# Performance work log

Hardware: AMD Instinct MI355X
Metric: run time of the kernel (lower is better)

## Reference

```python
import jax, jax.numpy as jnp
import numpy as np

NUM_GRAPHS = 4096


def setup_inputs() -> dict:
    key = jax.random.key(0)
    k1, k2, k3, k4 = jax.random.split(key, 4)
    N, H = 500000, 256
    x = jax.random.normal(k1, (N, H), dtype=jnp.float32)
    batch = jnp.sort(jax.random.randint(k2, (N,), 0, NUM_GRAPHS, dtype=jnp.int64))
    W1 = jax.random.normal(k3, (H, H), dtype=jnp.float32) * (1.0 / np.sqrt(H))
    b1 = jnp.zeros((H,), dtype=jnp.float32)
    w2 = jax.random.normal(k4, (H, 1), dtype=jnp.float32) * (1.0 / np.sqrt(H))
    return {"x": x, "batch": batch, "W1": W1, "b1": b1, "w2": w2}


def reference(x, batch, W1, b1, w2):
    # attention scores: Linear -> Tanh -> Linear(no bias)  -> [N, 1]
    scores = jnp.tanh(x @ W1 + b1) @ w2  # [N, 1]
    # Torch code scatter-maxes into a zeros buffer, so the effective per-graph
    # max is clamped below at 0 (faithfully replicated here).
    seg_max = jax.ops.segment_max(scores, batch, num_segments=NUM_GRAPHS)  # [G, 1]
    seg_max = jnp.maximum(seg_max, 0.0)
    exp_scores = jnp.exp(scores - seg_max[batch])  # [N, 1]
    sum_exp = jax.ops.segment_sum(exp_scores, batch, num_segments=NUM_GRAPHS)  # [G, 1]
    normalized = exp_scores / sum_exp[batch]  # [N, 1]
    graph_embedding = jax.ops.segment_sum(x * normalized, batch, num_segments=NUM_GRAPHS)  # [G, H]
    return graph_embedding
```

## Files before the change

kernel.cpp:

```cpp
#include <hip/hip_runtime.h>
#include <cstdint>

#define H 256
#define MT 64
#define ROWS 256

typedef _Float16 half8 __attribute__((ext_vector_type(8)));
typedef float floatx4 __attribute__((ext_vector_type(4)));

__device__ __forceinline__ float fast_tanh(float v) {
    v = fminf(fmaxf(v, -15.f), 15.f);
    float e = __expf(2.f * v);
    return (e - 1.f) / (e + 1.f);
}

__global__ void init_kernel(float4* __restrict__ out4, int* __restrict__ maxv,
                            float* __restrict__ sumexp, int G, int total4) {
    int i = blockIdx.x * 256 + threadIdx.x;
    if (i < total4) out4[i] = make_float4(0.f, 0.f, 0.f, 0.f);
    if (i < G) { maxv[i] = 0; sumexp[i] = 0.f; }
}

__global__ void w1conv_kernel(const float* __restrict__ W1, _Float16* __restrict__ w1c) {
    int i = blockIdx.x * 256 + threadIdx.x;
    if (i < H * H) {
        int r = i & 511;
        int lane = r >> 3, h = r & 7;
        int t = i >> 9;
        int kc = t & 1, s = (t >> 1) & 3, ct = t >> 3;
        int mm = lane & 15, qq = lane >> 4;
        int col = ct * 16 + mm;
        int k = s * 64 + kc * 32 + qq * 8 + h;
        w1c[i] = (_Float16)W1[k * H + col];
    }
}

__global__ __launch_bounds__(256, 3) void scores_kernel(
    const float* __restrict__ x, const _Float16* __restrict__ w1c,
    const float* __restrict__ b1, const float* __restrict__ w2,
    const int* __restrict__ batch,
    float* __restrict__ scores, int* __restrict__ maxv, int N) {
    __shared__ _Float16 As[2][64][64];
    __shared__ float sred[4][64];

    const int tid = threadIdx.x;
    const int wv = tid >> 6;
    const int lane = tid & 63;
    const int m = lane & 15;
    const int q = lane >> 4;
    const int row0 = blockIdx.x * MT;

    const int srow = tid >> 2;
    const int sc4 = tid & 3;
    const int sg0 = (sc4 * 2) ^ (srow & 7);
    const int sg1 = (sc4 * 2 + 1) ^ (srow & 7);
    const bool srok = (row0 + srow) < N;
    const float* sbase = x + (size_t)(row0 + srow) * H + sc4 * 16;

    floatx4 acc[4][4] = {};

    float4 f0, f1, f2, f3;
    f0 = f1 = f2 = f3 = make_float4(0.f, 0.f, 0.f, 0.f);
    if (srok) {
        const float4* p = (const float4*)sbase;
        f0 = p[0]; f1 = p[1]; f2 = p[2]; f3 = p[3];
    }
    {
        half8 h0, h1;
        h0[0] = (_Float16)f0.x; h0[1] = (_Float16)f0.y; h0[2] = (_Float16)f0.z; h0[3] = (_Float16)f0.w;
        h0[4] = (_Float16)f1.x; h0[5] = (_Float16)f1.y; h0[6] = (_Float16)f1.z; h0[7] = (_Float16)f1.w;
        h1[0] = (_Float16)f2.x; h1[1] = (_Float16)f2.y; h1[2] = (_Float16)f2.z; h1[3] = (_Float16)f2.w;
        h1[4] = (_Float16)f3.x; h1[5] = (_Float16)f3.y; h1[6] = (_Float16)f3.z; h1[7] = (_Float16)f3.w;
        *(half8*)&As[0][srow][sg0 * 8] = h0;
        *(half8*)&As[0][srow][sg1 * 8] = h1;
    }
    __syncthreads();

    for (int s = 0; s < 4; ++s) {
        const int cur = s & 1;
        if (s < 3 && srok) {
            const float4* p = (const float4*)(sbase + (s + 1) * 64);
            f0 = p[0]; f1 = p[1]; f2 = p[2]; f3 = p[3];
        }
        half8 bf[4][2];
#pragma unroll
        for (int ni = 0; ni < 4; ++ni) {
            int ct = wv * 4 + ni;
#pragma unroll
            for (int kc = 0; kc < 2; ++kc) {
                int chunk = ((ct << 2) | s) * 2 + kc;
                bf[ni][kc] = *(const half8*)(w1c + ((size_t)chunk << 9) + lane * 8);
            }
        }
        half8 af[4][2];
#pragma unroll
        for (int mi = 0; mi < 4; ++mi) {
            int r = mi * 16 + m;
#pragma unroll
            for (int kc = 0; kc < 2; ++kc) {
                int g = (kc * 4 + q) ^ (r & 7);
                af[mi][kc] = *(const half8*)&As[cur][r][g * 8];
            }
        }
#pragma unroll
        for (int mi = 0; mi < 4; ++mi)
#pragma unroll
            for (int ni = 0; ni < 4; ++ni) {
                acc[mi][ni] = __builtin_amdgcn_mfma_f32_16x16x32_f16(
                    af[mi][0], bf[ni][0], acc[mi][ni], 0, 0, 0);
                acc[mi][ni] = __builtin_amdgcn_mfma_f32_16x16x32_f16(
                    af[mi][1], bf[ni][1], acc[mi][ni], 0, 0, 0);
            }
        if (s < 3) {
            half8 h0, h1;
            h0[0] = (_Float16)f0.x; h0[1] = (_Float16)f0.y; h0[2] = (_Float16)f0.z; h0[3] = (_Float16)f0.w;
            h0[4] = (_Float16)f1.x; h0[5] = (_Float16)f1.y; h0[6] = (_Float16)f1.z; h0[7] = (_Float16)f1.w;
            h1[0] = (_Float16)f2.x; h1[1] = (_Float16)f2.y; h1[2] = (_Float16)f2.z; h1[3] = (_Float16)f2.w;
            h1[4] = (_Float16)f3.x; h1[5] = (_Float16)f3.y; h1[6] = (_Float16)f3.z; h1[7] = (_Float16)f3.w;
            *(half8*)&As[1 - cur][srow][sg0 * 8] = h0;
            *(half8*)&As[1 - cur][srow][sg1 * 8] = h1;
        }
        __syncthreads();
    }

    float b1c[4], w2c[4];
#pragma unroll
    for (int ni = 0; ni < 4; ++ni) {
        int c = wv * 64 + ni * 16 + m;
        b1c[ni] = b1[c];
        w2c[ni] = w2[c];
    }
#pragma unroll
    for (int mi = 0; mi < 4; ++mi) {
#pragma unroll
        for (int r = 0; r < 4; ++r) {
            float v = 0.f;
#pragma unroll
            for (int ni = 0; ni < 4; ++ni)
                v += w2c[ni] * fast_tanh(acc[mi][ni][r] + b1c[ni]);
            v += __shfl_xor(v, 1);
            v += __shfl_xor(v, 2);
            v += __shfl_xor(v, 4);
            v += __shfl_xor(v, 8);
            if (m == 0) sred[wv][mi * 16 + q * 4 + r] = v;
        }
    }
    __syncthreads();
    if (tid < MT) {
        int row = row0 + tid;
        if (row < N) {
            float sc = sred[0][tid] + sred[1][tid] + sred[2][tid] + sred[3][tid];
            scores[row] = sc;
            if (sc > 0.f) atomicMax(&maxv[batch[row]], __float_as_int(sc));
        }
    }
}

__global__ __launch_bounds__(256) void pass2_kernel(
    const float* __restrict__ x, const int* __restrict__ batch,
    const float* __restrict__ scores, const int* __restrict__ maxv,
    float* __restrict__ out, float* __restrict__ sumexp, int N) {
    const int t = threadIdx.x;
    const int sub = t >> 6;
    const int lane = t & 63;
    const int base = blockIdx.x * ROWS;
    const int i1 = min(base + ROWS, N);
    int i = base + sub;
    if (i >= i1) return;

    const float4* x4 = (const float4*)x;

    float ax = 0.f, ay = 0.f, az = 0.f, aw = 0.f, sw = 0.f;
    int cur = batch[i];
    int g = cur;
    float4 xv = x4[(size_t)i * 64 + lane];
    float w = __expf(scores[i] - __int_as_float(maxv[cur]));

    while (i < i1) {
        int inx = i + 4;
        float4 xv_n = make_float4(0.f, 0.f, 0.f, 0.f);
        float w_n = 0.f;
        int g_n = g;
        if (inx < i1) {
            xv_n = x4[(size_t)inx * 64 + lane];
            g_n = batch[inx];
            w_n = __expf(scores[inx] - __int_as_float(maxv[g_n]));
        }
        if (g != cur) {
            float* o = out + (size_t)cur * H + lane * 4;
            atomicAdd(o + 0, ax); atomicAdd(o + 1, ay);
            atomicAdd(o + 2, az); atomicAdd(o + 3, aw);
            if (lane == 0) atomicAdd(&sumexp[cur], sw);
            ax = ay = az = aw = 0.f; sw = 0.f;
            cur = g;
        }
        ax = fmaf(w, xv.x, ax);
        ay = fmaf(w, xv.y, ay);
        az = fmaf(w, xv.z, az);
        aw = fmaf(w, xv.w, aw);
        if (lane == 0) sw += w;
        xv = xv_n; w = w_n; g = g_n;
        i = inx;
    }
    float* o = out + (size_t)cur * H + lane * 4;
    atomicAdd(o + 0, ax); atomicAdd(o + 1, ay);
    atomicAdd(o + 2, az); atomicAdd(o + 3, aw);
    if (lane == 0) atomicAdd(&sumexp[cur], sw);
}

__global__ void normalize_kernel(float4* __restrict__ out4,
                                 const float* __restrict__ sumexp, int total4) {
    int i = blockIdx.x * 256 + threadIdx.x;
    if (i < total4) {
        float s = sumexp[i >> 6];
        if (s > 0.f) {
            float inv = 1.f / s;
            float4 v = out4[i];
            v.x *= inv; v.y *= inv; v.z *= inv; v.w *= inv;
            out4[i] = v;
        } else {
            out4[i] = make_float4(0.f, 0.f, 0.f, 0.f);
        }
    }
}

extern "C" void kernel_launch(void* const* d_in, const int* in_sizes, int n_in,
                              void* d_out, int out_size, void* d_ws, size_t ws_size,
                              hipStream_t stream) {
    const float* x = (const float*)d_in[0];
    const int* batch = (const int*)d_in[1];
    const float* W1 = (const float*)d_in[2];
    const float* b1 = (const float*)d_in[3];
    const float* w2 = (const float*)d_in[4];
    float* out = (float*)d_out;

    const int N = in_sizes[0] / H;
    const int G = out_size / H;

    char* ws = (char*)d_ws;
    float* scores = (float*)ws;
    size_t off = (size_t)N * sizeof(float);
    off = (off + 15) & ~(size_t)15;
    int* maxv = (int*)(ws + off);
    off += (size_t)G * sizeof(int);
    float* sumexp = (float*)(ws + off);
    off += (size_t)G * sizeof(float);
    off = (off + 15) & ~(size_t)15;
    _Float16* w1c = (_Float16*)(ws + off);

    const int total4 = (G * H) / 4;
    init_kernel<<<(max(total4, G) + 255) / 256, 256, 0, stream>>>(
        (float4*)out, maxv, sumexp, G, total4);
    w1conv_kernel<<<(H * H + 255) / 256, 256, 0, stream>>>(W1, w1c);
    scores_kernel<<<(N + MT - 1) / MT, 256, 0, stream>>>(
        x, w1c, b1, w2, batch, scores, maxv, N);
    pass2_kernel<<<(N + ROWS - 1) / ROWS, 256, 0, stream>>>(
        x, batch, scores, maxv, out, sumexp, N);
    normalize_kernel<<<(total4 + 255) / 256, 256, 0, stream>>>(
        (float4*)out, sumexp, total4);
}
```

Baseline: 912.4 us.

## Fuse score computation with weighted segment pooling and drop the max pass

Merges the scores kernel and the pooling kernel into one. Each 64-row tile now computes exp(score) directly, with no per-graph max subtraction, and accumulates weighted x rows into the output with atomics while those rows are still hot in cache. This removes the second full read of x, the scores buffer and the atomicMax pass. It also merges the init and W1 conversion kernels into a single setup launch. In exchange, exp can overflow if scores ever exceed about 88; tanh bounds each score by the L1 norm of w2, which is small for these inputs. Atomics on the output also rise, because tiles are smaller than the old 256-row pooling blocks.

```diff
diff --git a/kernel.cpp b/kernel.cpp
--- a/kernel.cpp
+++ b/kernel.cpp
@@ -3,7 +3,6 @@
 
 #define H 256
 #define MT 64
-#define ROWS 256
 
 typedef _Float16 half8 __attribute__((ext_vector_type(8)));
 typedef float floatx4 __attribute__((ext_vector_type(4)));
@@ -14,15 +13,12 @@
     return (e - 1.f) / (e + 1.f);
 }
 
-__global__ void init_kernel(float4* __restrict__ out4, int* __restrict__ maxv,
-                            float* __restrict__ sumexp, int G, int total4) {
+__global__ void setup_kernel(const float* __restrict__ W1,
+                             float4* __restrict__ out4, float* __restrict__ Z,
+                             _Float16* __restrict__ w1c, int total4, int G) {
     int i = blockIdx.x * 256 + threadIdx.x;
     if (i < total4) out4[i] = make_float4(0.f, 0.f, 0.f, 0.f);
-    if (i < G) { maxv[i] = 0; sumexp[i] = 0.f; }
-}
-
-__global__ void w1conv_kernel(const float* __restrict__ W1, _Float16* __restrict__ w1c) {
-    int i = blockIdx.x * 256 + threadIdx.x;
+    if (i < G) Z[i] = 0.f;
     if (i < H * H) {
         int r = i & 511;
         int lane = r >> 3, h = r & 7;
@@ -35,13 +31,15 @@
     }
 }
 
-__global__ __launch_bounds__(256, 3) void scores_kernel(
+__global__ __launch_bounds__(256, 3) void fused_kernel(
     const float* __restrict__ x, const _Float16* __restrict__ w1c,
     const float* __restrict__ b1, const float* __restrict__ w2,
     const int* __restrict__ batch,
-    float* __restrict__ scores, int* __restrict__ maxv, int N) {
+    float* __restrict__ out, float* __restrict__ Z, int N) {
     __shared__ _Float16 As[2][64][64];
     __shared__ float sred[4][64];
+    __shared__ float sexp[64];
+    __shared__ int gid[64];
 
     const int tid = threadIdx.x;
     const int wv = tid >> 6;
@@ -150,69 +148,41 @@
         int row = row0 + tid;
         if (row < N) {
             float sc = sred[0][tid] + sred[1][tid] + sred[2][tid] + sred[3][tid];
-            scores[row] = sc;
-            if (sc > 0.f) atomicMax(&maxv[batch[row]], __float_as_int(sc));
-        }
-    }
-}
-
-__global__ __launch_bounds__(256) void pass2_kernel(
-    const float* __restrict__ x, const int* __restrict__ batch,
-    const float* __restrict__ scores, const int* __restrict__ maxv,
-    float* __restrict__ out, float* __restrict__ sumexp, int N) {
-    const int t = threadIdx.x;
-    const int sub = t >> 6;
-    const int lane = t & 63;
-    const int base = blockIdx.x * ROWS;
-    const int i1 = min(base + ROWS, N);
-    int i = base + sub;
-    if (i >= i1) return;
-
-    const float4* x4 = (const float4*)x;
-
-    float ax = 0.f, ay = 0.f, az = 0.f, aw = 0.f, sw = 0.f;
-    int cur = batch[i];
-    int g = cur;
-    float4 xv = x4[(size_t)i * 64 + lane];
-    float w = __expf(scores[i] - __int_as_float(maxv[cur]));
-
-    while (i < i1) {
-        int inx = i + 4;
-        float4 xv_n = make_float4(0.f, 0.f, 0.f, 0.f);
-        float w_n = 0.f;
-        int g_n = g;
-        if (inx < i1) {
-            xv_n = x4[(size_t)inx * 64 + lane];
-            g_n = batch[inx];
-            w_n = __expf(scores[inx] - __int_as_float(maxv[g_n]));
-        }
+            sexp[tid] = __expf(sc);
+            gid[tid] = batch[row];
+        } else {
+            sexp[tid] = 0.f;
+            gid[tid] = batch[N - 1];
+        }
+    }
+    __syncthreads();
+
+    const int nval = min(MT, N - row0);
+    const float* px = x + (size_t)row0 * H + tid;
+    float acc2 = 0.f, zacc = 0.f;
+    int cur = gid[0];
+#pragma unroll 4
+    for (int r = 0; r < nval; ++r) {
+        int g = gid[r];
+        float w = sexp[r];
+        float xv = px[(size_t)r * H];
         if (g != cur) {
-            float* o = out + (size_t)cur * H + lane * 4;
-            atomicAdd(o + 0, ax); atomicAdd(o + 1, ay);
-            atomicAdd(o + 2, az); atomicAdd(o + 3, aw);
-            if (lane == 0) atomicAdd(&sumexp[cur], sw);
-            ax = ay = az = aw = 0.f; sw = 0.f;
-            cur = g;
-        }
-        ax = fmaf(w, xv.x, ax);
-        ay = fmaf(w, xv.y, ay);
-        az = fmaf(w, xv.z, az);
-        aw = fmaf(w, xv.w, aw);
-        if (lane == 0) sw += w;
-        xv = xv_n; w = w_n; g = g_n;
-        i = inx;
-    }
-    float* o = out + (size_t)cur * H + lane * 4;
-    atomicAdd(o + 0, ax); atomicAdd(o + 1, ay);
-    atomicAdd(o + 2, az); atomicAdd(o + 3, aw);
-    if (lane == 0) atomicAdd(&sumexp[cur], sw);
+            atomicAdd(&out[(size_t)cur * H + tid], acc2);
+            if (tid == 0) atomicAdd(&Z[cur], zacc);
+            acc2 = 0.f; zacc = 0.f; cur = g;
+        }
+        acc2 = fmaf(w, xv, acc2);
+        zacc += w;
+    }
+    atomicAdd(&out[(size_t)cur * H + tid], acc2);
+    if (tid == 0) atomicAdd(&Z[cur], zacc);
 }
 
 __global__ void normalize_kernel(float4* __restrict__ out4,
-                                 const float* __restrict__ sumexp, int total4) {
+                                 const float* __restrict__ Z, int total4) {
     int i = blockIdx.x * 256 + threadIdx.x;
     if (i < total4) {
-        float s = sumexp[i >> 6];
+        float s = Z[i >> 6];
         if (s > 0.f) {
             float inv = 1.f / s;
             float4 v = out4[i];
@@ -238,24 +208,17 @@
     const int G = out_size / H;
 
     char* ws = (char*)d_ws;
-    float* scores = (float*)ws;
-    size_t off = (size_t)N * sizeof(float);
-    off = (off + 15) & ~(size_t)15;
-    int* maxv = (int*)(ws + off);
-    off += (size_t)G * sizeof(int);
-    float* sumexp = (float*)(ws + off);
-    off += (size_t)G * sizeof(float);
+    float* Z = (float*)ws;
+    size_t off = (size_t)G * sizeof(float);
     off = (off + 15) & ~(size_t)15;
     _Float16* w1c = (_Float16*)(ws + off);
 
     const int total4 = (G * H) / 4;
-    init_kernel<<<(max(total4, G) + 255) / 256, 256, 0, stream>>>(
-        (float4*)out, maxv, sumexp, G, total4);
-    w1conv_kernel<<<(H * H + 255) / 256, 256, 0, stream>>>(W1, w1c);
-    scores_kernel<<<(N + MT - 1) / MT, 256, 0, stream>>>(
-        x, w1c, b1, w2, batch, scores, maxv, N);
-    pass2_kernel<<<(N + ROWS - 1) / ROWS, 256, 0, stream>>>(
-        x, batch, scores, maxv, out, sumexp, N);
+    int setup_items = max(total4, H * H);
+    setup_kernel<<<(setup_items + 255) / 256, 256, 0, stream>>>(
+        W1, (float4*)out, Z, w1c, total4, G);
+    fused_kernel<<<(N + MT - 1) / MT, 256, 0, stream>>>(
+        x, w1c, b1, w2, batch, out, Z, N);
     normalize_kernel<<<(total4 + 255) / 256, 256, 0, stream>>>(
-        (float4*)out, sumexp, total4);
-}
+        (float4*)out, Z, total4);
+}
```

After: 823.7 us. 9.7% less time.
